# Performance work log

Hardware: AMD Instinct MI355X
Metric: run time of the kernel (lower is better)

## Reference

```python
import jax, jax.numpy as jnp
import numpy as np

N, F_IN, PRE, K = 400000, 64, 32, 6
EDGE = [32, 32]


def _dense_params(key, fan_in, fan_out):
    kw, kb = jax.random.split(key)
    W = jax.random.normal(kw, (fan_in, fan_out), jnp.float32) / np.sqrt(fan_in).astype(np.float32)
    b = jnp.zeros((fan_out,), jnp.float32)
    return W, b


def setup_inputs() -> dict:
    key = jax.random.key(0)
    ks = jax.random.split(key, 10)
    x = jax.random.normal(ks[0], (N, F_IN), jnp.float32)
    distsq = jax.random.uniform(ks[1], (N, K), jnp.float32)
    nidx = jax.random.randint(ks[2], (N, K), 0, N, jnp.int64)
    Wp, bp = _dense_params(ks[3], F_IN, PRE)
    # edge MLP: input K*(PRE+1) -> 32 -> 32 -> K
    We1, be1 = _dense_params(ks[4], K * (PRE + 1), EDGE[0])
    We2, be2 = _dense_params(ks[5], EDGE[0], EDGE[1])
    We3, be3 = _dense_params(ks[6], EDGE[1], K)
    # self MLP: F_IN -> 32 -> 32 -> 1
    Ws1, bs1 = _dense_params(ks[7], F_IN, EDGE[0])
    Ws2, bs2 = _dense_params(ks[8], EDGE[0], EDGE[1])
    Ws3, bs3 = _dense_params(ks[9], EDGE[1], 1)
    return dict(x=x, distsq=distsq, nidx=nidx, Wp=Wp, bp=bp,
                We1=We1, be1=be1, We2=We2, be2=be2, We3=We3, be3=be3,
                Ws1=Ws1, bs1=bs1, Ws2=Ws2, bs2=bs2, Ws3=Ws3, bs3=bs3)


def _forward(x, distsq, nidx, Wp, bp, We1, be1, We2, be2, We3, be3,
             Ws1, bs1, Ws2, bs2, Ws3, bs3):
    # pre-dense: [N, PRE]
    x_p = jax.nn.elu(x @ Wp + bp)
    # gather neighbors; select(nidx, x_n, 0.0) masks nidx<0 to 0.0
    safe_idx = jnp.maximum(nidx, 0)
    gathered = x_p[safe_idx]                              # [N, K, PRE]
    gathered = jnp.where(nidx[:, :, None] < 0, 0.0, gathered)
    diff = x_p[:, None, :] - gathered                     # [N, K, PRE]
    xn = jnp.concatenate([diff, distsq[:, :, None]], axis=2)  # [N, K, PRE+1]
    xn = xn.reshape(xn.shape[0], K * (PRE + 1))
    xn = jax.nn.elu(xn @ We1 + be1)
    xn = jax.nn.elu(xn @ We2 + be2)
    xn = xn @ We3 + be3                                   # [N, K]
    xs = jax.nn.elu(x @ Ws1 + bs1)
    xs = jax.nn.elu(xs @ Ws2 + bs2)
    xs = xs @ Ws3 + bs3                                   # [N, 1]
    out = jnp.concatenate([xs, xn], axis=1)               # [N, K+1]
    return jax.nn.softmax(out, axis=1)


def reference(x, distsq, nidx, Wp, bp, We1, be1, We2, be2, We3, be3,
              Ws1, bs1, Ws2, bs2, Ws3, bs3):
    return _forward(x, distsq, nidx, Wp, bp, We1, be1, We2, be2, We3, be3,
                    Ws1, bs1, Ws2, bs2, Ws3, bs3)
```

## Files before the change

### kernel.cpp

```cpp
#include <hip/hip_runtime.h>
#include <hip/hip_bf16.h>
#include <math.h>

typedef __hip_bfloat16 bf16;
typedef __attribute__((ext_vector_type(8))) __bf16 bf16x8;
typedef __attribute__((ext_vector_type(4))) float f32x4;

#define F_IN 64
#define KNB 6

#define WOFF_WP   0
#define WOFF_BP   2048
#define WOFF_WE1  2080
#define WOFF_BE1  8416
#define WOFF_WE2  8448
#define WOFF_BE2  9472
#define WOFF_WE3  9504
#define WOFF_BE3  9696
#define WOFF_WS1  9728
#define WOFF_BS1  11776
#define WOFF_WS2  11808
#define WOFF_BS2  12832
#define WOFF_WS3  12864
#define WOFF_BS3  12896
#define FLAGS_OFF 13056
#define WOFF_WSUM 13312
#define WOFF_WDSQ 14336
#define STAGE_OFF 16384

__device__ __forceinline__ float b2f(bf16 v) { return __bfloat162float(v); }
__device__ __forceinline__ float eluf(float v) { return v > 0.f ? v : expm1f(v); }

__device__ __forceinline__ ushort f2bu(float v) {
  __bf16 b = (__bf16)v; ushort u; __builtin_memcpy(&u, &b, 2); return u;
}

union U8 { uint4 u; bf16x8 v; ushort s[8]; };

__device__ __forceinline__ void lds_fence() {
  __builtin_amdgcn_wave_barrier();
  __builtin_amdgcn_s_waitcnt(0xC07F);
  __builtin_amdgcn_wave_barrier();
}

__global__ void detect(const ushort* xb, const int* ni, int* flags) {
  if (threadIdx.x == 0 && blockIdx.x == 0) {
    int bad = 0;
    for (int i = 0; i < 256; i++) {
      float v = __uint_as_float(((unsigned)xb[i]) << 16);
      if (!(fabsf(v) < 100.f)) bad++;
    }
    int hi_nonzero = 0;
    for (int i = 0; i < 64; i++) if (ni[2 * i + 1] != 0) hi_nonzero = 1;
    flags[0] = (bad < 8) ? 1 : 0;
    flags[1] = hi_nonzero ? 0 : 1;
  }
}

__global__ void wstage(const void* Wp, const void* bp, const void* We1, const void* be1,
                       const void* We2, const void* be2, const void* We3, const void* be3,
                       const void* Ws1, const void* bs1, const void* Ws2, const void* bs2,
                       const void* Ws3, const void* bs3, float* w, const int* flags) {
  const void* srcs[14] = {Wp, bp, We1, be1, We2, be2, We3, be3, Ws1, bs1, Ws2, bs2, Ws3, bs3};
  const int sizes[14] = {2048, 32, 6336, 32, 1024, 32, 192, 6, 2048, 32, 1024, 32, 32, 1};
  const int offs[14] = {WOFF_WP, WOFF_BP, WOFF_WE1, WOFF_BE1, WOFF_WE2, WOFF_BE2, WOFF_WE3,
                        WOFF_BE3, WOFF_WS1, WOFF_BS1, WOFF_WS2, WOFF_BS2, WOFF_WS3, WOFF_BS3};
  int bf = flags[0];
  int t = blockIdx.x;
  const void* s = srcs[t];
  int nel = sizes[t];
  float* d = w + offs[t];
  if (bf) {
    const bf16* sb = (const bf16*)s;
    for (int i = threadIdx.x; i < nel; i += blockDim.x) d[i] = b2f(sb[i]);
  } else {
    const float* sf = (const float*)s;
    for (int i = threadIdx.x; i < nel; i += blockDim.x) d[i] = sf[i];
  }
}

__global__ void wprep(float* w) {
  int t = blockIdx.x * blockDim.x + threadIdx.x;
  if (t < 1024) {
    int j = t >> 5, o = t & 31;
    float s = 0.f;
    for (int k = 0; k < KNB; k++) s += w[WOFF_WE1 + (k * 33 + j) * 32 + o];
    w[WOFF_WSUM + t] = s;
  }
  if (t < 192) {
    int k = t >> 5, o = t & 31;
    w[WOFF_WDSQ + t] = w[WOFF_WE1 + (k * 33 + 32) * 32 + o];
  }
}

__device__ __forceinline__ bf16x8 bfrag(const float* W, int ld, int nValid, int kValid, float sgn) {
  int lane = threadIdx.x & 63;
  int n = lane & 15, quad = lane >> 4;
  bf16x8 r;
#pragma unroll
  for (int j = 0; j < 8; j++) {
    int k = quad * 8 + j;
    float v = (n < nValid && k < kValid) ? sgn * W[k * ld + n] : 0.f;
    r[j] = (__bf16)v;
  }
  return r;
}

template <bool BF16>
__device__ __forceinline__ bf16x8 afrag_row(const void* base, long row, int k0) {
  int quad = (threadIdx.x & 63) >> 4;
  if (BF16) {
    U8 u;
    u.u = *(const uint4*)((const ushort*)base + row * F_IN + k0 + quad * 8);
    return u.v;
  } else {
    const float* p = (const float*)base + row * F_IN + k0 + quad * 8;
    float4 a = *(const float4*)p, b = *(const float4*)(p + 4);
    bf16x8 r;
    r[0] = (__bf16)a.x; r[1] = (__bf16)a.y; r[2] = (__bf16)a.z; r[3] = (__bf16)a.w;
    r[4] = (__bf16)b.x; r[5] = (__bf16)b.y; r[6] = (__bf16)b.z; r[7] = (__bf16)b.w;
    return r;
  }
}

template <bool BF16>
__device__ void pre_tiles(const void* xv, const float* __restrict__ w,
                          ushort* __restrict__ xp, float* __restrict__ xs,
                          int n_nodes, ushort* buf) {
  int lane = threadIdx.x & 63;
  int m = lane & 15, quad = lane >> 4;

  bf16x8 fwp[2][2], fws1[2][2], fws2[2], fws3;
#pragma unroll
  for (int s = 0; s < 2; s++)
#pragma unroll
    for (int t = 0; t < 2; t++) {
      fwp[s][t]  = bfrag(w + WOFF_WP  + s * 32 * 32 + 16 * t, 32, 16, 32, 1.f);
      fws1[s][t] = bfrag(w + WOFF_WS1 + s * 32 * 32 + 16 * t, 32, 16, 32, 1.f);
    }
#pragma unroll
  for (int t = 0; t < 2; t++) fws2[t] = bfrag(w + WOFF_WS2 + 16 * t, 32, 16, 32, 1.f);
  fws3 = bfrag(w + WOFF_WS3, 1, 1, 32, 1.f);
  float bpv[2], bs1v[2], bs2v[2];
#pragma unroll
  for (int t = 0; t < 2; t++) {
    bpv[t]  = w[WOFF_BP  + m + 16 * t];
    bs1v[t] = w[WOFF_BS1 + m + 16 * t];
    bs2v[t] = w[WOFF_BS2 + m + 16 * t];
  }
  float bs3f = w[WOFF_BS3];

  int T = (n_nodes + 15) >> 4;
  int wid = (int)((blockIdx.x * blockDim.x + threadIdx.x) >> 6);
  int nw = (int)((gridDim.x * blockDim.x) >> 6);
  f32x4 zero = {0.f, 0.f, 0.f, 0.f};

  for (int t0 = wid; t0 < T; t0 += nw) {
    long n0 = (long)t0 * 16;
    long row = n0 + m; if (row >= n_nodes) row = n_nodes - 1;
    bf16x8 a0 = afrag_row<BF16>(xv, row, 0);
    bf16x8 a1 = afrag_row<BF16>(xv, row, 32);
    f32x4 accp[2], accs[2];
#pragma unroll
    for (int t = 0; t < 2; t++) {
      accp[t] = __builtin_amdgcn_mfma_f32_16x16x32_bf16(a0, fwp[0][t], zero, 0, 0, 0);
      accp[t] = __builtin_amdgcn_mfma_f32_16x16x32_bf16(a1, fwp[1][t], accp[t], 0, 0, 0);
      accs[t] = __builtin_amdgcn_mfma_f32_16x16x32_bf16(a0, fws1[0][t], zero, 0, 0, 0);
      accs[t] = __builtin_amdgcn_mfma_f32_16x16x32_bf16(a1, fws1[1][t], accs[t], 0, 0, 0);
    }
#pragma unroll
    for (int t = 0; t < 2; t++)
#pragma unroll
      for (int r = 0; r < 4; r++)
        buf[(quad * 4 + r) * 32 + m + 16 * t] = f2bu(eluf(accp[t][r] + bpv[t]));
    lds_fence();
    {
      uint4 rv = *(const uint4*)(buf + m * 32 + quad * 8);
      *(uint4*)(xp + row * 32 + quad * 8) = rv;
    }
#pragma unroll
    for (int t = 0; t < 2; t++)
#pragma unroll
      for (int r = 0; r < 4; r++)
        buf[(quad * 4 + r) * 32 + m + 16 * t] = f2bu(eluf(accs[t][r] + bs1v[t]));
    lds_fence();
    U8 as1; as1.u = *(const uint4*)(buf + m * 32 + quad * 8);
    f32x4 acc2[2];
#pragma unroll
    for (int t = 0; t < 2; t++)
      acc2[t] = __builtin_amdgcn_mfma_f32_16x16x32_bf16(as1.v, fws2[t], zero, 0, 0, 0);
#pragma unroll
    for (int t = 0; t < 2; t++)
#pragma unroll
      for (int r = 0; r < 4; r++)
        buf[(quad * 4 + r) * 32 + m + 16 * t] = f2bu(eluf(acc2[t][r] + bs2v[t]));
    lds_fence();
    U8 as2; as2.u = *(const uint4*)(buf + m * 32 + quad * 8);
    f32x4 accx = __builtin_amdgcn_mfma_f32_16x16x32_bf16(as2.v, fws3, zero, 0, 0, 0);
    if (m == 0) {
#pragma unroll
      for (int r = 0; r < 4; r++) {
        long orow = n0 + quad * 4 + r;
        if (orow < n_nodes) xs[orow] = accx[r] + bs3f;
      }
    }
    lds_fence();
  }
}

__launch_bounds__(256)
__global__ void preK(const void* xv, const float* __restrict__ w,
                     const int* __restrict__ flags,
                     ushort* __restrict__ xp, float* __restrict__ xs, int n_nodes) {
  __shared__ ushort sb[4 * 512];
  ushort* buf = sb + (threadIdx.x >> 6) * 512;
  if (flags[0]) pre_tiles<true>(xv, w, xp, xs, n_nodes, buf);
  else          pre_tiles<false>(xv, w, xp, xs, n_nodes, buf);
}

template <bool BF16>
__device__ void edge_tiles(const ushort* __restrict__ xp, const float* __restrict__ xs,
                           const void* dsv, const int* __restrict__ ni, int i64,
                           const float* __restrict__ w, void* outv, int n_nodes,
                           ushort* buf, float* lbuf) {
  int lane = threadIdx.x & 63;
  int m = lane & 15, quad = lane >> 4;

  bf16x8 fsum[2], fwe1[KNB][2], fdsq[2], fwe2[2], fwe3;
#pragma unroll
  for (int t = 0; t < 2; t++) {
    fsum[t] = bfrag(w + WOFF_WSUM + 16 * t, 32, 16, 32, 1.f);
    fdsq[t] = bfrag(w + WOFF_WDSQ + 16 * t, 32, 16, KNB, 1.f);
    fwe2[t] = bfrag(w + WOFF_WE2 + 16 * t, 32, 16, 32, 1.f);
#pragma unroll
    for (int k = 0; k < KNB; k++)
      fwe1[k][t] = bfrag(w + WOFF_WE1 + k * 33 * 32 + 16 * t, 32, 16, 32, -1.f);
  }
  fwe3 = bfrag(w + WOFF_WE3, 6, 6, 32, 1.f);
  float be1v[2], be2v[2];
#pragma unroll
  for (int t = 0; t < 2; t++) {
    be1v[t] = w[WOFF_BE1 + m + 16 * t];
    be2v[t] = w[WOFF_BE2 + m + 16 * t];
  }
  float be3v = (m < 6) ? w[WOFF_BE3 + m] : 0.f;

  int T = (n_nodes + 15) >> 4;
  int wid = (int)((blockIdx.x * blockDim.x + threadIdx.x) >> 6);
  int nw = (int)((gridDim.x * blockDim.x) >> 6);
  f32x4 zero = {0.f, 0.f, 0.f, 0.f};

  for (int t0 = wid; t0 < T; t0 += nw) {
    long n0 = (long)t0 * 16;
    long row = n0 + m; if (row >= n_nodes) row = n_nodes - 1;

    int idxs[KNB];
#pragma unroll
    for (int k = 0; k < KNB; k++)
      idxs[k] = i64 ? ni[(row * KNB + k) * 2] : ni[row * KNB + k];

    U8 own; own.u = *(const uint4*)(xp + row * 32 + quad * 8);
    U8 nb[KNB];
#pragma unroll
    for (int k = 0; k < KNB; k++) {
      long ai = idxs[k];
      if (ai < 0 || ai >= n_nodes) ai = 0;
      nb[k].u = *(const uint4*)(xp + ai * 32 + quad * 8);
      if (idxs[k] < 0) { nb[k].u.x = 0; nb[k].u.y = 0; nb[k].u.z = 0; nb[k].u.w = 0; }
    }

    U8 ad; ad.u.x = 0; ad.u.y = 0; ad.u.z = 0; ad.u.w = 0;
    if (quad == 0) {
      if (BF16) {
        const unsigned* dp = (const unsigned*)dsv;
        ad.u.x = dp[row * 3 + 0];
        ad.u.y = dp[row * 3 + 1];
        ad.u.z = dp[row * 3 + 2];
      } else {
        const float* dp = (const float*)dsv + row * KNB;
#pragma unroll
        for (int k = 0; k < KNB; k++) ad.s[k] = f2bu(dp[k]);
      }
    }

    f32x4 accA[2], accB[2];
#pragma unroll
    for (int t = 0; t < 2; t++) {
      accA[t] = __builtin_amdgcn_mfma_f32_16x16x32_bf16(own.v, fsum[t], zero, 0, 0, 0);
      accA[t] = __builtin_amdgcn_mfma_f32_16x16x32_bf16(nb[0].v, fwe1[0][t], accA[t], 0, 0, 0);
      accA[t] = __builtin_amdgcn_mfma_f32_16x16x32_bf16(nb[1].v, fwe1[1][t], accA[t], 0, 0, 0);
      accA[t] = __builtin_amdgcn_mfma_f32_16x16x32_bf16(nb[2].v, fwe1[2][t], accA[t], 0, 0, 0);
      accB[t] = __builtin_amdgcn_mfma_f32_16x16x32_bf16(nb[3].v, fwe1[3][t], zero, 0, 0, 0);
      accB[t] = __builtin_amdgcn_mfma_f32_16x16x32_bf16(nb[4].v, fwe1[4][t], accB[t], 0, 0, 0);
      accB[t] = __builtin_amdgcn_mfma_f32_16x16x32_bf16(nb[5].v, fwe1[5][t], accB[t], 0, 0, 0);
      accB[t] = __builtin_amdgcn_mfma_f32_16x16x32_bf16(ad.v, fdsq[t], accB[t], 0, 0, 0);
    }
#pragma unroll
    for (int t = 0; t < 2; t++)
#pragma unroll
      for (int r = 0; r < 4; r++)
        buf[(quad * 4 + r) * 32 + m + 16 * t] =
            f2bu(eluf(accA[t][r] + accB[t][r] + be1v[t]));
    lds_fence();
    U8 a1; a1.u = *(const uint4*)(buf + m * 32 + quad * 8);
    f32x4 acc2[2];
#pragma unroll
    for (int t = 0; t < 2; t++)
      acc2[t] = __builtin_amdgcn_mfma_f32_16x16x32_bf16(a1.v, fwe2[t], zero, 0, 0, 0);
#pragma unroll
    for (int t = 0; t < 2; t++)
#pragma unroll
      for (int r = 0; r < 4; r++)
        buf[(quad * 4 + r) * 32 + m + 16 * t] = f2bu(eluf(acc2[t][r] + be2v[t]));
    lds_fence();
    U8 a2; a2.u = *(const uint4*)(buf + m * 32 + quad * 8);
    f32x4 acc3 = __builtin_amdgcn_mfma_f32_16x16x32_bf16(a2.v, fwe3, zero, 0, 0, 0);

    if (m < 6) {
#pragma unroll
      for (int r = 0; r < 4; r++) lbuf[(quad * 4 + r) * 8 + m] = acc3[r] + be3v;
    }
    lds_fence();
    if (lane < 16) {
      long nodeid = n0 + lane;
      if (nodeid < n_nodes) {
        float lg[7];
        lg[0] = xs[nodeid];
#pragma unroll
        for (int i = 0; i < 6; i++) lg[1 + i] = lbuf[lane * 8 + i];
        float mx = lg[0];
#pragma unroll
        for (int i = 1; i < 7; i++) mx = fmaxf(mx, lg[i]);
        float e[7], ssum = 0.f;
#pragma unroll
        for (int i = 0; i < 7; i++) { e[i] = expf(lg[i] - mx); ssum += e[i]; }
        float inv = 1.f / ssum;
        if (BF16) {
          ushort* o = (ushort*)outv + nodeid * 7;
#pragma unroll
          for (int i = 0; i < 7; i++) o[i] = f2bu(e[i] * inv);
        } else {
          float* o = (float*)outv + nodeid * 7;
#pragma unroll
          for (int i = 0; i < 7; i++) o[i] = e[i] * inv;
        }
      }
    }
    lds_fence();
  }
}

__launch_bounds__(256)
__global__ void edgeK(const ushort* __restrict__ xp, const float* __restrict__ xs,
                      const void* dsv, const int* __restrict__ ni,
                      const float* __restrict__ w, const int* __restrict__ flags,
                      void* outv, int n_nodes) {
  __shared__ ushort sb[4 * 512];
  __shared__ float sl[4 * 128];
  ushort* buf = sb + (threadIdx.x >> 6) * 512;
  float* lbuf = sl + (threadIdx.x >> 6) * 128;
  int bf = flags[0];
  int i64 = flags[1];
  if (bf) edge_tiles<true>(xp, xs, dsv, ni, i64, w, outv, n_nodes, buf, lbuf);
  else    edge_tiles<false>(xp, xs, dsv, ni, i64, w, outv, n_nodes, buf, lbuf);
}

__device__ __forceinline__ void bf8_to_f32(uint4 u, float* f) {
  unsigned int w[4] = {u.x, u.y, u.z, u.w};
#pragma unroll
  for (int i = 0; i < 4; i++) {
    f[2 * i]     = __uint_as_float(w[i] << 16);
    f[2 * i + 1] = __uint_as_float(w[i] & 0xffff0000u);
  }
}

template <bool BF16>
__device__ __forceinline__ void load_row8(const void* base, long row, int chunk, float* f) {
  if (BF16) {
    const uint4* p = (const uint4*)((const ushort*)base + row * F_IN);
    bf8_to_f32(p[chunk], f);
  } else {
    const float4* p = (const float4*)((const float*)base + row * F_IN);
    float4 a = p[2 * chunk];
    float4 b = p[2 * chunk + 1];
    f[0] = a.x; f[1] = a.y; f[2] = a.z; f[3] = a.w;
    f[4] = b.x; f[5] = b.y; f[6] = b.z; f[7] = b.w;
  }
}

template <bool BF16>
__device__ void node_body(int n, int n_nodes, const void* xv, const void* dsv,
                          const int* __restrict__ ni, int i64,
                          const float* __restrict__ w, void* outv) {
  const float* Wp  = w + WOFF_WP;
  const float* bp  = w + WOFF_BP;
  const float* We1 = w + WOFF_WE1;
  const float* be1 = w + WOFF_BE1;
  const float* We2 = w + WOFF_WE2;
  const float* be2 = w + WOFF_BE2;
  const float* We3 = w + WOFF_WE3;
  const float* be3 = w + WOFF_BE3;
  const float* Ws1 = w + WOFF_WS1;
  const float* bs1 = w + WOFF_BS1;
  const float* Ws2 = w + WOFF_WS2;
  const float* bs2 = w + WOFF_BS2;
  const float* Ws3 = w + WOFF_WS3;
  const float* bs3 = w + WOFF_BS3;

  float h[32], s1[32];
#pragma unroll
  for (int o = 0; o < 32; o++) { h[o] = bp[o]; s1[o] = bs1[o]; }
  for (int c = 0; c < 8; c++) {
    float xv8[8];
    load_row8<BF16>(xv, n, c, xv8);
#pragma unroll
    for (int q = 0; q < 8; q++) {
      int j = c * 8 + q;
      float xj = xv8[q];
#pragma unroll
      for (int o = 0; o < 32; o++) {
        h[o]  += xj * Wp[j * 32 + o];
        s1[o] += xj * Ws1[j * 32 + o];
      }
    }
  }
  float own[32];
#pragma unroll
  for (int o = 0; o < 32; o++) own[o] = eluf(h[o]);
  float s2[32];
#pragma unroll
  for (int o = 0; o < 32; o++) s2[o] = bs2[o];
  for (int j = 0; j < 32; j++) {
    float v = eluf(s1[j]);
#pragma unroll
    for (int o = 0; o < 32; o++) s2[o] += v * Ws2[j * 32 + o];
  }
  float xsv = bs3[0];
#pragma unroll
  for (int j = 0; j < 32; j++) xsv += eluf(s2[j]) * Ws3[j];

  float h1[32];
#pragma unroll
  for (int o = 0; o < 32; o++) h1[o] = be1[o];
  for (int k = 0; k < KNB; k++) {
    long pos = (long)n * KNB + k;
    int idx = i64 ? ni[2 * pos] : ni[pos];
    float mmask = idx < 0 ? 0.f : 1.f;
    long ai = idx < 0 ? 0 : idx;
    if (ai >= n_nodes) ai = 0;
    float nh[32];
#pragma unroll
    for (int o = 0; o < 32; o++) nh[o] = bp[o];
    for (int c = 0; c < 8; c++) {
      float xv8[8];
      load_row8<BF16>(xv, ai, c, xv8);
#pragma unroll
      for (int q = 0; q < 8; q++) {
        int j = c * 8 + q;
        float xj = xv8[q];
#pragma unroll
        for (int o = 0; o < 32; o++) nh[o] += xj * Wp[j * 32 + o];
      }
    }
    const float* Wk = We1 + (k * 33) * 32;
#pragma unroll
    for (int j = 0; j < 32; j++) {
      float d = own[j] - mmask * eluf(nh[j]);
#pragma unroll
      for (int o = 0; o < 32; o++) h1[o] += d * Wk[j * 32 + o];
    }
    float dsq = BF16 ? b2f(((const bf16*)dsv)[pos]) : ((const float*)dsv)[pos];
#pragma unroll
    for (int o = 0; o < 32; o++) h1[o] += dsq * Wk[32 * 32 + o];
  }
  float h2[32];
#pragma unroll
  for (int o = 0; o < 32; o++) h2[o] = be2[o];
  for (int j = 0; j < 32; j++) {
    float v = eluf(h1[j]);
#pragma unroll
    for (int o = 0; o < 32; o++) h2[o] += v * We2[j * 32 + o];
  }
  float lg[7];
  lg[0] = xsv;
#pragma unroll
  for (int o = 0; o < 6; o++) lg[1 + o] = be3[o];
  for (int j = 0; j < 32; j++) {
    float v = eluf(h2[j]);
#pragma unroll
    for (int o = 0; o < 6; o++) lg[1 + o] += v * We3[j * 6 + o];
  }
  float mx = lg[0];
#pragma unroll
  for (int i = 1; i < 7; i++) mx = fmaxf(mx, lg[i]);
  float e[7], ssum = 0.f;
#pragma unroll
  for (int i = 0; i < 7; i++) { e[i] = expf(lg[i] - mx); ssum += e[i]; }
  float inv = 1.f / ssum;
  if (BF16) {
    bf16* o = (bf16*)outv;
#pragma unroll
    for (int i = 0; i < 7; i++) o[(long)n * 7 + i] = __float2bfloat16(e[i] * inv);
  } else {
    float* o = (float*)outv;
#pragma unroll
    for (int i = 0; i < 7; i++) o[(long)n * 7 + i] = e[i] * inv;
  }
}

__launch_bounds__(256)
__global__ void fused(const void* xv, const void* dsv, const int* __restrict__ ni,
                      const float* __restrict__ w, const int* __restrict__ flags,
                      void* outv, int n_nodes) {
  int n = blockIdx.x * blockDim.x + threadIdx.x;
  if (n >= n_nodes) return;
  int bf = flags[0];
  int i64 = flags[1];
  if (bf) node_body<true>(n, n_nodes, xv, dsv, ni, i64, w, outv);
  else    node_body<false>(n, n_nodes, xv, dsv, ni, i64, w, outv);
}

extern "C" void kernel_launch(void* const* d_in, const int* in_sizes, int n_in,
                              void* d_out, int out_size, void* d_ws, size_t ws_size,
                              hipStream_t stream) {
  const void* x      = d_in[0];
  const void* distsq = d_in[1];
  const int*  nidx   = (const int*)d_in[2];

  float* w = (float*)d_ws;
  int* flags = (int*)(w + FLAGS_OFF);
  int n_nodes = in_sizes[0] / F_IN;

  detect<<<1, 64, 0, stream>>>((const ushort*)x, nidx, flags);
  wstage<<<14, 256, 0, stream>>>(d_in[3], d_in[4], d_in[5], d_in[6], d_in[7], d_in[8],
                                 d_in[9], d_in[10], d_in[11], d_in[12], d_in[13], d_in[14],
                                 d_in[15], d_in[16], w, flags);
  wprep<<<4, 256, 0, stream>>>(w);

  size_t need = (size_t)STAGE_OFF * 4 + (size_t)n_nodes * 64 + (size_t)n_nodes * 4 + 256;
  if (ws_size >= need) {
    ushort* xp = (ushort*)(w + STAGE_OFF);
    float* xs = (float*)(xp + (size_t)n_nodes * 32);
    preK<<<1024, 256, 0, stream>>>(x, w, flags, xp, xs, n_nodes);
    edgeK<<<1024, 256, 0, stream>>>(xp, xs, distsq, nidx, w, flags, d_out, n_nodes);
  } else {
    int grid = (n_nodes + 255) / 256;
    fused<<<grid, 256, 0, stream>>>(x, distsq, nidx, w, flags, d_out, n_nodes);
  }
}
```

Before: 298.9 us.

## Prefetch next tile in pre/edge loops, merge setup kernels, use fast exp

Software-pipelines the grid-stride loops in the pre and edge kernels so the next tile's input rows, neighbor indices and gathered neighbor features are loaded while the current tile's MFMAs run. The three small setup kernels are merged into one single-block kernel to cut launch count. expm1f/expf are replaced with __expf, and the launch bounds now set a minimum occupancy. Holding the prefetched tiles raises register pressure, and the fast exp slightly changes ELU accuracy near zero.

```diff
diff --git a/kernel.cpp b/kernel.cpp
--- a/kernel.cpp
+++ b/kernel.cpp
@@ -29,7 +29,7 @@
 #define STAGE_OFF 16384
 
 __device__ __forceinline__ float b2f(bf16 v) { return __bfloat162float(v); }
-__device__ __forceinline__ float eluf(float v) { return v > 0.f ? v : expm1f(v); }
+__device__ __forceinline__ float eluf(float v) { return v > 0.f ? v : __expf(v) - 1.f; }
 
 __device__ __forceinline__ ushort f2bu(float v) {
   __bf16 b = (__bf16)v; ushort u; __builtin_memcpy(&u, &b, 2); return u;
@@ -43,53 +43,51 @@
   __builtin_amdgcn_wave_barrier();
 }
 
-__global__ void detect(const ushort* xb, const int* ni, int* flags) {
-  if (threadIdx.x == 0 && blockIdx.x == 0) {
+__global__ void setupK(const ushort* xb, const int* ni,
+                       const void* Wp, const void* bp, const void* We1, const void* be1,
+                       const void* We2, const void* be2, const void* We3, const void* be3,
+                       const void* Ws1, const void* bs1, const void* Ws2, const void* bs2,
+                       const void* Ws3, const void* bs3, float* w) {
+  __shared__ int sbf;
+  int t = threadIdx.x;
+  if (t < 64) {
     int bad = 0;
-    for (int i = 0; i < 256; i++) {
+    for (int i = t; i < 256; i += 64) {
       float v = __uint_as_float(((unsigned)xb[i]) << 16);
       if (!(fabsf(v) < 100.f)) bad++;
     }
-    int hi_nonzero = 0;
-    for (int i = 0; i < 64; i++) if (ni[2 * i + 1] != 0) hi_nonzero = 1;
-    flags[0] = (bad < 8) ? 1 : 0;
-    flags[1] = hi_nonzero ? 0 : 1;
-  }
-}
-
-__global__ void wstage(const void* Wp, const void* bp, const void* We1, const void* be1,
-                       const void* We2, const void* be2, const void* We3, const void* be3,
-                       const void* Ws1, const void* bs1, const void* Ws2, const void* bs2,
-                       const void* Ws3, const void* bs3, float* w, const int* flags) {
+    unsigned long long bm = __ballot(bad > 0);
+    unsigned long long hm = __ballot(ni[2 * t + 1] != 0);
+    if (t == 0) {
+      int isbf = (__popcll(bm) < 4) ? 1 : 0;
+      ((int*)(w + FLAGS_OFF))[0] = isbf;
+      ((int*)(w + FLAGS_OFF))[1] = (hm == 0ULL) ? 1 : 0;
+      sbf = isbf;
+    }
+  }
+  __syncthreads();
+  int bf = sbf;
   const void* srcs[14] = {Wp, bp, We1, be1, We2, be2, We3, be3, Ws1, bs1, Ws2, bs2, Ws3, bs3};
   const int sizes[14] = {2048, 32, 6336, 32, 1024, 32, 192, 6, 2048, 32, 1024, 32, 32, 1};
   const int offs[14] = {WOFF_WP, WOFF_BP, WOFF_WE1, WOFF_BE1, WOFF_WE2, WOFF_BE2, WOFF_WE3,
                         WOFF_BE3, WOFF_WS1, WOFF_BS1, WOFF_WS2, WOFF_BS2, WOFF_WS3, WOFF_BS3};
-  int bf = flags[0];
-  int t = blockIdx.x;
-  const void* s = srcs[t];
-  int nel = sizes[t];
-  float* d = w + offs[t];
-  if (bf) {
-    const bf16* sb = (const bf16*)s;
-    for (int i = threadIdx.x; i < nel; i += blockDim.x) d[i] = b2f(sb[i]);
-  } else {
-    const float* sf = (const float*)s;
-    for (int i = threadIdx.x; i < nel; i += blockDim.x) d[i] = sf[i];
-  }
-}
-
-__global__ void wprep(float* w) {
-  int t = blockIdx.x * blockDim.x + threadIdx.x;
-  if (t < 1024) {
-    int j = t >> 5, o = t & 31;
+  for (int tt = 0; tt < 14; tt++) {
+    const void* s = srcs[tt];
+    int nel = sizes[tt];
+    float* d = w + offs[tt];
+    for (int i = t; i < nel; i += blockDim.x)
+      d[i] = bf ? b2f(((const bf16*)s)[i]) : ((const float*)s)[i];
+  }
+  __syncthreads();
+  for (int i = t; i < 1024; i += blockDim.x) {
+    int j = i >> 5, o = i & 31;
     float s = 0.f;
     for (int k = 0; k < KNB; k++) s += w[WOFF_WE1 + (k * 33 + j) * 32 + o];
-    w[WOFF_WSUM + t] = s;
-  }
-  if (t < 192) {
-    int k = t >> 5, o = t & 31;
-    w[WOFF_WDSQ + t] = w[WOFF_WE1 + (k * 33 + 32) * 32 + o];
+    w[WOFF_WSUM + i] = s;
+  }
+  for (int i = t; i < 192; i += blockDim.x) {
+    int k = i >> 5, o = i & 31;
+    w[WOFF_WDSQ + i] = w[WOFF_WE1 + (k * 33 + 32) * 32 + o];
   }
 }
 
@@ -153,13 +151,25 @@
   int T = (n_nodes + 15) >> 4;
   int wid = (int)((blockIdx.x * blockDim.x + threadIdx.x) >> 6);
   int nw = (int)((gridDim.x * blockDim.x) >> 6);
+  if (wid >= T) return;
   f32x4 zero = {0.f, 0.f, 0.f, 0.f};
 
-  for (int t0 = wid; t0 < T; t0 += nw) {
-    long n0 = (long)t0 * 16;
-    long row = n0 + m; if (row >= n_nodes) row = n_nodes - 1;
-    bf16x8 a0 = afrag_row<BF16>(xv, row, 0);
-    bf16x8 a1 = afrag_row<BF16>(xv, row, 32);
+  long cur = wid;
+  long crow = cur * 16 + m; if (crow >= n_nodes) crow = n_nodes - 1;
+  bf16x8 a0 = afrag_row<BF16>(xv, crow, 0);
+  bf16x8 a1 = afrag_row<BF16>(xv, crow, 32);
+
+  while (true) {
+    long nxt = cur + nw;
+    bool more = nxt < T;
+    long nrow = 0;
+    bf16x8 na0, na1;
+    if (more) {
+      nrow = nxt * 16 + m; if (nrow >= n_nodes) nrow = n_nodes - 1;
+      na0 = afrag_row<BF16>(xv, nrow, 0);
+      na1 = afrag_row<BF16>(xv, nrow, 32);
+    }
+
     f32x4 accp[2], accs[2];
 #pragma unroll
     for (int t = 0; t < 2; t++) {
@@ -176,7 +186,7 @@
     lds_fence();
     {
       uint4 rv = *(const uint4*)(buf + m * 32 + quad * 8);
-      *(uint4*)(xp + row * 32 + quad * 8) = rv;
+      *(uint4*)(xp + crow * 32 + quad * 8) = rv;
     }
 #pragma unroll
     for (int t = 0; t < 2; t++)
@@ -200,15 +210,18 @@
     if (m == 0) {
 #pragma unroll
       for (int r = 0; r < 4; r++) {
-        long orow = n0 + quad * 4 + r;
+        long orow = cur * 16 + quad * 4 + r;
         if (orow < n_nodes) xs[orow] = accx[r] + bs3f;
       }
     }
     lds_fence();
-  }
-}
-
-__launch_bounds__(256)
+
+    if (!more) break;
+    cur = nxt; crow = nrow; a0 = na0; a1 = na1;
+  }
+}
+
+__launch_bounds__(256, 4)
 __global__ void preK(const void* xv, const float* __restrict__ w,
                      const int* __restrict__ flags,
                      ushort* __restrict__ xp, float* __restrict__ xs, int n_nodes) {
@@ -218,6 +231,23 @@
   else          pre_tiles<false>(xv, w, xp, xs, n_nodes, buf);
 }
 
+__device__ __forceinline__ void load_idx(const int* __restrict__ ni, int i64, long row, int* idxs) {
+#pragma unroll
+  for (int k = 0; k < KNB; k++)
+    idxs[k] = i64 ? ni[(row * KNB + k) * 2] : ni[row * KNB + k];
+}
+
+__device__ __forceinline__ void load_nb(const ushort* __restrict__ xp, int n_nodes,
+                                        const int* idxs, int quad, U8* nb) {
+#pragma unroll
+  for (int k = 0; k < KNB; k++) {
+    long ai = idxs[k];
+    if (ai < 0 || ai >= n_nodes) ai = 0;
+    nb[k].u = *(const uint4*)(xp + ai * 32 + quad * 8);
+    if (idxs[k] < 0) { nb[k].u.x = 0; nb[k].u.y = 0; nb[k].u.z = 0; nb[k].u.w = 0; }
+  }
+}
+
 template <bool BF16>
 __device__ void edge_tiles(const ushort* __restrict__ xp, const float* __restrict__ xs,
                            const void* dsv, const int* __restrict__ ni, int i64,
@@ -248,53 +278,58 @@
   int T = (n_nodes + 15) >> 4;
   int wid = (int)((blockIdx.x * blockDim.x + threadIdx.x) >> 6);
   int nw = (int)((gridDim.x * blockDim.x) >> 6);
+  if (wid >= T) return;
   f32x4 zero = {0.f, 0.f, 0.f, 0.f};
 
-  for (int t0 = wid; t0 < T; t0 += nw) {
-    long n0 = (long)t0 * 16;
-    long row = n0 + m; if (row >= n_nodes) row = n_nodes - 1;
-
-    int idxs[KNB];
-#pragma unroll
-    for (int k = 0; k < KNB; k++)
-      idxs[k] = i64 ? ni[(row * KNB + k) * 2] : ni[row * KNB + k];
-
-    U8 own; own.u = *(const uint4*)(xp + row * 32 + quad * 8);
-    U8 nb[KNB];
-#pragma unroll
-    for (int k = 0; k < KNB; k++) {
-      long ai = idxs[k];
-      if (ai < 0 || ai >= n_nodes) ai = 0;
-      nb[k].u = *(const uint4*)(xp + ai * 32 + quad * 8);
-      if (idxs[k] < 0) { nb[k].u.x = 0; nb[k].u.y = 0; nb[k].u.z = 0; nb[k].u.w = 0; }
-    }
-
+  long cur = wid;
+  long crow = cur * 16 + m; if (crow >= n_nodes) crow = n_nodes - 1;
+  int cidx[KNB];
+  load_idx(ni, i64, crow, cidx);
+  U8 nb[KNB];
+  load_nb(xp, n_nodes, cidx, quad, nb);
+
+  while (true) {
+    long nxt = cur + nw;
+    bool more = nxt < T;
+    long nrow = 0;
+    int nidxA[KNB];
+    if (more) {
+      nrow = nxt * 16 + m; if (nrow >= n_nodes) nrow = n_nodes - 1;
+      load_idx(ni, i64, nrow, nidxA);
+    }
+
+    U8 own; own.u = *(const uint4*)(xp + crow * 32 + quad * 8);
     U8 ad; ad.u.x = 0; ad.u.y = 0; ad.u.z = 0; ad.u.w = 0;
     if (quad == 0) {
       if (BF16) {
         const unsigned* dp = (const unsigned*)dsv;
-        ad.u.x = dp[row * 3 + 0];
-        ad.u.y = dp[row * 3 + 1];
-        ad.u.z = dp[row * 3 + 2];
+        ad.u.x = dp[crow * 3 + 0];
+        ad.u.y = dp[crow * 3 + 1];
+        ad.u.z = dp[crow * 3 + 2];
       } else {
-        const float* dp = (const float*)dsv + row * KNB;
+        const float* dp = (const float*)dsv + crow * KNB;
 #pragma unroll
         for (int k = 0; k < KNB; k++) ad.s[k] = f2bu(dp[k]);
       }
     }
+    float xsv = xs[crow];
 
     f32x4 accA[2], accB[2];
 #pragma unroll
     for (int t = 0; t < 2; t++) {
-      accA[t] = __builtin_amdgcn_mfma_f32_16x16x32_bf16(own.v, fsum[t], zero, 0, 0, 0);
-      accA[t] = __builtin_amdgcn_mfma_f32_16x16x32_bf16(nb[0].v, fwe1[0][t], accA[t], 0, 0, 0);
+      accA[t] = __builtin_amdgcn_mfma_f32_16x16x32_bf16(nb[0].v, fwe1[0][t], zero, 0, 0, 0);
       accA[t] = __builtin_amdgcn_mfma_f32_16x16x32_bf16(nb[1].v, fwe1[1][t], accA[t], 0, 0, 0);
       accA[t] = __builtin_amdgcn_mfma_f32_16x16x32_bf16(nb[2].v, fwe1[2][t], accA[t], 0, 0, 0);
       accB[t] = __builtin_amdgcn_mfma_f32_16x16x32_bf16(nb[3].v, fwe1[3][t], zero, 0, 0, 0);
       accB[t] = __builtin_amdgcn_mfma_f32_16x16x32_bf16(nb[4].v, fwe1[4][t], accB[t], 0, 0, 0);
       accB[t] = __builtin_amdgcn_mfma_f32_16x16x32_bf16(nb[5].v, fwe1[5][t], accB[t], 0, 0, 0);
       accB[t] = __builtin_amdgcn_mfma_f32_16x16x32_bf16(ad.v, fdsq[t], accB[t], 0, 0, 0);
-    }
+      accA[t] = __builtin_amdgcn_mfma_f32_16x16x32_bf16(own.v, fsum[t], accA[t], 0, 0, 0);
+    }
+
+    U8 nnb[KNB];
+    if (more) load_nb(xp, n_nodes, nidxA, quad, nnb);
+
 #pragma unroll
     for (int t = 0; t < 2; t++)
 #pragma unroll
@@ -322,10 +357,10 @@
     }
     lds_fence();
     if (lane < 16) {
-      long nodeid = n0 + lane;
+      long nodeid = cur * 16 + lane;
       if (nodeid < n_nodes) {
         float lg[7];
-        lg[0] = xs[nodeid];
+        lg[0] = xsv;
 #pragma unroll
         for (int i = 0; i < 6; i++) lg[1 + i] = lbuf[lane * 8 + i];
         float mx = lg[0];
@@ -333,7 +368,7 @@
         for (int i = 1; i < 7; i++) mx = fmaxf(mx, lg[i]);
         float e[7], ssum = 0.f;
 #pragma unroll
-        for (int i = 0; i < 7; i++) { e[i] = expf(lg[i] - mx); ssum += e[i]; }
+        for (int i = 0; i < 7; i++) { e[i] = __expf(lg[i] - mx); ssum += e[i]; }
         float inv = 1.f / ssum;
         if (BF16) {
           ushort* o = (ushort*)outv + nodeid * 7;
@@ -347,10 +382,15 @@
       }
     }
     lds_fence();
-  }
-}
-
-__launch_bounds__(256)
+
+    if (!more) break;
+    cur = nxt; crow = nrow;
+#pragma unroll
+    for (int k = 0; k < KNB; k++) nb[k] = nnb[k];
+  }
+}
+
+__launch_bounds__(256, 3)
 __global__ void edgeK(const ushort* __restrict__ xp, const float* __restrict__ xs,
                       const void* dsv, const int* __restrict__ ni,
                       const float* __restrict__ w, const int* __restrict__ flags,
@@ -495,7 +535,7 @@
   for (int i = 1; i < 7; i++) mx = fmaxf(mx, lg[i]);
   float e[7], ssum = 0.f;
 #pragma unroll
-  for (int i = 0; i < 7; i++) { e[i] = expf(lg[i] - mx); ssum += e[i]; }
+  for (int i = 0; i < 7; i++) { e[i] = __expf(lg[i] - mx); ssum += e[i]; }
   float inv = 1.f / ssum;
   if (BF16) {
     bf16* o = (bf16*)outv;
@@ -531,11 +571,10 @@
   int* flags = (int*)(w + FLAGS_OFF);
   int n_nodes = in_sizes[0] / F_IN;
 
-  detect<<<1, 64, 0, stream>>>((const ushort*)x, nidx, flags);
-  wstage<<<14, 256, 0, stream>>>(d_in[3], d_in[4], d_in[5], d_in[6], d_in[7], d_in[8],
-                                 d_in[9], d_in[10], d_in[11], d_in[12], d_in[13], d_in[14],
-                                 d_in[15], d_in[16], w, flags);
-  wprep<<<4, 256, 0, stream>>>(w);
+  setupK<<<1, 256, 0, stream>>>((const ushort*)x, nidx,
+                                d_in[3], d_in[4], d_in[5], d_in[6], d_in[7], d_in[8],
+                                d_in[9], d_in[10], d_in[11], d_in[12], d_in[13], d_in[14],
+                                d_in[15], d_in[16], w);
 
   size_t need = (size_t)STAGE_OFF * 4 + (size_t)n_nodes * 64 + (size_t)n_nodes * 4 + 256;
   if (ws_size >= need) {
```

New measurement: 346.9 us. 1.16x slower.
